# Optimization experiments

Measured on AMD Instinct MI355X. Metric: run time of the kernel, lower is better.

The kernel has to match this reference:

```python
import jax, jax.numpy as jnp
import numpy as np

Q, N_EMBED, DIM = 4, 1024, 256
B, S = 8, 2048


def setup_inputs() -> dict:
    key = jax.random.key(0)
    k1, k2 = jax.random.split(key)
    x = jax.random.normal(k1, (B, S, DIM), dtype=jnp.float32)
    codebooks = jax.random.normal(k2, (Q, N_EMBED, DIM), dtype=jnp.float32)
    return {"x": x, "codebooks": codebooks}


def _vq_lookup(flat, embed):
    # flat: [M, D], embed: [K, D]
    dist = (jnp.sum(flat * flat, axis=-1, keepdims=True)
            - 2.0 * flat @ embed.T
            + jnp.sum(embed * embed, axis=-1))
    idx = jnp.argmin(dist, axis=-1)          # [M]
    quantize = embed[idx]                    # gather: [M, D]
    return quantize, idx


def reference(x, codebooks):
    sg = jax.lax.stop_gradient
    b, s, d = x.shape
    num_q = codebooks.shape[0]
    residual = x
    quantized_output = jnp.zeros_like(x)
    all_indices, all_losses = [], []
    for i in range(num_q):  # small fixed loop over quantizers
        flat = residual.reshape(-1, d)
        q, idx = _vq_lookup(flat, codebooks[i])
        q = q.reshape(b, s, d)
        # commitment loss: mse(sg(quantize), input)
        loss = jnp.mean((sg(q) - residual) ** 2)
        # straight-through estimator
        q_st = residual + sg(q - residual)
        residual = residual - q_st
        quantized_output = quantized_output + q_st
        all_indices.append(idx.reshape(b, s))
        all_losses.append(loss)
    return quantized_output, jnp.stack(all_indices), jnp.stack(all_losses)
```

## Files before the change

kernel.cpp:

```cpp
#include <hip/hip_runtime.h>

#define QQ   4
#define NE   1024
#define DIMD 256
#define MM   16384
#define TM   32
#define NW   8
#define CAP  32

typedef short v8s __attribute__((ext_vector_type(8)));
typedef float v4f __attribute__((ext_vector_type(4)));


__device__ __forceinline__ unsigned short f2bf(float f) {
  unsigned u = __float_as_uint(f);
  return (unsigned short)((u + 0x7FFFu + ((u >> 16) & 1u)) >> 16);
}

__device__ __forceinline__ float np_sumsq_256_x32(const float* __restrict__ p,
                                                  int j) {
  const int bi = j >> 4, L = j & 15;
  const float* q = p + bi * 128 + L;
  float s0 = __fmul_rn(q[0], q[0]);
  float s1 = __fmul_rn(q[16], q[16]);
  float s2 = __fmul_rn(q[32], q[32]);
  float s3 = __fmul_rn(q[48], q[48]);
  float s4 = __fmul_rn(q[64], q[64]);
  float s5 = __fmul_rn(q[80], q[80]);
  float s6 = __fmul_rn(q[96], q[96]);
  float s7 = __fmul_rn(q[112], q[112]);
  float w = __fadd_rn(__fadd_rn(__fadd_rn(s0, s1), __fadd_rn(s2, s3)),
                      __fadd_rn(__fadd_rn(s4, s5), __fadd_rn(s6, s7)));
  float u  = __fadd_rn(w,  __shfl_down(w, 8, 64));
  float t  = __fadd_rn(u,  __shfl_down(u, 4, 64));
  float r2 = __fadd_rn(t,  __shfl_down(t, 2, 64));
  float bb = __fadd_rn(r2, __shfl_down(r2, 1, 64));
  return __fadd_rn(bb, __shfl_down(bb, 16, 64));
}

__device__ __forceinline__ float np_sumsq_256_x16(const float* __restrict__ p,
                                                  int j) {
  float blk[2];
  #pragma unroll
  for (int bi = 0; bi < 2; ++bi) {
    const float* q = p + bi * 128 + j;
    float s0 = __fmul_rn(q[0], q[0]);
    float s1 = __fmul_rn(q[16], q[16]);
    float s2 = __fmul_rn(q[32], q[32]);
    float s3 = __fmul_rn(q[48], q[48]);
    float s4 = __fmul_rn(q[64], q[64]);
    float s5 = __fmul_rn(q[80], q[80]);
    float s6 = __fmul_rn(q[96], q[96]);
    float s7 = __fmul_rn(q[112], q[112]);
    float w = __fadd_rn(__fadd_rn(__fadd_rn(s0, s1), __fadd_rn(s2, s3)),
                        __fadd_rn(__fadd_rn(s4, s5), __fadd_rn(s6, s7)));
    float u  = __fadd_rn(w,  __shfl_down(w, 8, 64));
    float t  = __fadd_rn(u,  __shfl_down(u, 4, 64));
    float r2 = __fadd_rn(t,  __shfl_down(t, 2, 64));
    blk[bi]  = __fadd_rn(r2, __shfl_down(r2, 1, 64));
  }
  return __fadd_rn(blk[0], blk[1]);
}

__device__ __forceinline__ float np_dist_f4(const float* __restrict__ xp,
                                            const float* __restrict__ ep,
                                            float a, float b) {
  float m = 0.f;
  #pragma unroll 16
  for (int d4 = 0; d4 < DIMD / 4; ++d4) {
    const float4 xv = *(const float4*)(xp + d4 * 4);
    const float4 ev = *(const float4*)(ep + d4 * 4);
    m = fmaf(xv.x, ev.x, m);
    m = fmaf(xv.y, ev.y, m);
    m = fmaf(xv.z, ev.z, m);
    m = fmaf(xv.w, ev.w, m);
  }
  return __fadd_rn(__fsub_rn(a, __fmul_rn(2.0f, m)), b);
}

__global__ __launch_bounds__(256) void k_prep(const float* __restrict__ cb,
                                              unsigned short* __restrict__ cb16,
                                              float* __restrict__ bK,
                                              double* __restrict__ lossP,
                                              unsigned* __restrict__ done) {
  const int g = blockIdx.x * 256 + threadIdx.x;
  {
    const int i = g * 4;
    float4 f = *(const float4*)(cb + i);
    unsigned short t[4] = {f2bf(f.x), f2bf(f.y), f2bf(f.z), f2bf(f.w)};
    *(short4*)(cb16 + i) = *(short4*)t;
  }
  if (g < QQ * NE * 32) {
    const int row = g >> 5, j = g & 31;
    float b = np_sumsq_256_x32(cb + (size_t)row * DIMD, j);
    if (j == 0) bK[row] = b;
  }
  if (g < QQ * 64) lossP[g] = 0.0;
  if (g == 0) *done = 0u;
}

__global__ __launch_bounds__(512, 2) void k_fused(
    const float* __restrict__ x,
    const unsigned short* __restrict__ cb16a,
    const float* __restrict__ cba,
    const float* __restrict__ bKa,
    double* __restrict__ lossP,
    unsigned* __restrict__ doneCnt,
    float* __restrict__ out_q,
    float* __restrict__ idx_out,
    float* __restrict__ out_loss) {
  __shared__ float residF[TM][DIMD + 4];
  __shared__ unsigned short sX[TM][DIMD + 8];
  __shared__ float  sBK[NE];
  __shared__ float  av_s[TM];
  __shared__ float  candD[TM][NW];
  __shared__ float  thrS[TM];
  __shared__ int    cnt[TM];
  __shared__ int    candL[TM][CAP];
  __shared__ float  dcD[TM][CAP];
  __shared__ int    bcode[TM];
  __shared__ float  fwD[NW];
  __shared__ int    fwI[NW];
  __shared__ double lossW[NW];

  const int tid  = threadIdx.x;
  const int lane = tid & 63;
  const int wv   = tid >> 6;
  const int rowBase = blockIdx.x * TM;
  const int r16 = tid >> 4;
  const int j16 = tid & 15;
  const int d0  = j16 * 16;
  const int m16  = lane & 15;
  const int quad = lane >> 4;

  {
    const float* xp = x + (size_t)(rowBase + r16) * DIMD + d0;
    #pragma unroll
    for (int h = 0; h < 4; ++h)
      *(float4*)&residF[r16][d0 + h * 4] = *(const float4*)(xp + h * 4);
  }
  __syncthreads();

  #pragma unroll 1
  for (int qi = 0; qi < QQ; ++qi) {
    const unsigned short* cb16 = cb16a + (size_t)qi * NE * DIMD;
    const float* cb = cba + (size_t)qi * NE * DIMD;
    const float* bK = bKa + (size_t)qi * NE;

    {
      float av = np_sumsq_256_x16(&residF[r16][0], j16);
      if (j16 == 0) av_s[r16] = av;
    }
    if (tid < TM) cnt[tid] = 0;
    sBK[tid] = bK[tid];
    sBK[tid + 512] = bK[tid + 512];
    {
      #pragma unroll
      for (int h = 0; h < 2; ++h) {
        const float* rp = &residF[r16][d0 + h * 8];
        const float4 f0 = *(const float4*)rp;
        const float4 f1 = *(const float4*)(rp + 4);
        unsigned short t[8] = {f2bf(f0.x), f2bf(f0.y), f2bf(f0.z), f2bf(f0.w),
                               f2bf(f1.x), f2bf(f1.y), f2bf(f1.z), f2bf(f1.w)};
        *(v8s*)&sX[r16][d0 + h * 8] = *(v8s*)t;
      }
    }
    __syncthreads();

    float bmx;
    {
      float bm = sBK[lane];
      #pragma unroll
      for (int t = 1; t < 16; ++t) bm = fmaxf(bm, sBK[lane + t * 64]);
      #pragma unroll
      for (int off = 32; off; off >>= 1) bm = fmaxf(bm, __shfl_xor(bm, off, 64));
      bmx = bm;
    }

    v4f acc[2][8];
    #pragma unroll
    for (int mt = 0; mt < 2; ++mt)
      #pragma unroll
      for (int ct = 0; ct < 8; ++ct) acc[mt][ct] = (v4f)(0.f);
    const unsigned short* bptr =
        cb16 + ((size_t)(wv * 128 + m16)) * DIMD + quad * 8;
    #pragma unroll
    for (int kc = 0; kc < 8; ++kc) {
      v8s bfr[8];
      #pragma unroll
      for (int ct = 0; ct < 8; ++ct)
        bfr[ct] = *(const v8s*)(bptr + (size_t)ct * 16 * DIMD + kc * 32);
      v8s a0 = *(const v8s*)&sX[m16][kc * 32 + quad * 8];
      v8s a1 = *(const v8s*)&sX[16 + m16][kc * 32 + quad * 8];
      #pragma unroll
      for (int ct = 0; ct < 8; ++ct) {
        acc[0][ct] = __builtin_amdgcn_mfma_f32_16x16x32_bf16(a0, bfr[ct], acc[0][ct], 0, 0, 0);
        acc[1][ct] = __builtin_amdgcn_mfma_f32_16x16x32_bf16(a1, bfr[ct], acc[1][ct], 0, 0, 0);
      }
    }

    float av8[2][4];
    #pragma unroll
    for (int mt = 0; mt < 2; ++mt)
      #pragma unroll
      for (int v = 0; v < 4; ++v) av8[mt][v] = av_s[mt * 16 + quad * 4 + v];
    #pragma unroll
    for (int ct = 0; ct < 8; ++ct) {
      const float bv = sBK[wv * 128 + ct * 16 + m16];
      #pragma unroll
      for (int mt = 0; mt < 2; ++mt)
        #pragma unroll
        for (int v = 0; v < 4; ++v)
          acc[mt][ct][v] = av8[mt][v] - 2.0f * acc[mt][ct][v] + bv;
    }

    #pragma unroll
    for (int mt = 0; mt < 2; ++mt) {
      float vmin[4];
      #pragma unroll
      for (int v = 0; v < 4; ++v) {
        vmin[v] = acc[mt][0][v];
        #pragma unroll
        for (int ct = 1; ct < 8; ++ct) vmin[v] = fminf(vmin[v], acc[mt][ct][v]);
        #pragma unroll
        for (int off = 1; off < 16; off <<= 1)
          vmin[v] = fminf(vmin[v], __shfl_xor(vmin[v], off, 64));
      }
      if (m16 == 0) {
        #pragma unroll
        for (int v = 0; v < 4; ++v) candD[mt * 16 + quad * 4 + v][wv] = vmin[v];
      }
    }
    __syncthreads();
    if (tid < TM) {
      float bd = candD[tid][0];
      #pragma unroll
      for (int w = 1; w < NW; ++w) bd = fminf(bd, candD[tid][w]);
      thrS[tid] = bd + 0.03125f * sqrtf(av_s[tid] * bmx) + 0.1f;
    }
    __syncthreads();

    #pragma unroll
    for (int ct = 0; ct < 8; ++ct) {
      const int code = wv * 128 + ct * 16 + m16;
      #pragma unroll
      for (int mt = 0; mt < 2; ++mt) {
        #pragma unroll
        for (int v = 0; v < 4; ++v) {
          const int row = mt * 16 + quad * 4 + v;
          if (acc[mt][ct][v] <= thrS[row]) {
            int pos = atomicAdd(&cnt[row], 1);
            if (pos < CAP) candL[row][pos] = code;
          }
        }
      }
    }
    __syncthreads();

    {
      const int n = (cnt[r16] <= CAP) ? cnt[r16] : 0;
      if (j16 < n) {
        const int code = candL[r16][j16];
        dcD[r16][j16] = np_dist_f4(&residF[r16][0], cb + (size_t)code * DIMD,
                                   av_s[r16], sBK[code]);
      }
      if (j16 + 16 < n) {
        const int code = candL[r16][j16 + 16];
        dcD[r16][j16 + 16] = np_dist_f4(&residF[r16][0], cb + (size_t)code * DIMD,
                                        av_s[r16], sBK[code]);
      }
    }
    __syncthreads();

    for (int r = 0; r < TM; ++r) {
      if (cnt[r] > CAP) {
        const float* xp = &residF[r][0];
        const float a = av_s[r];
        float d1 = np_dist_f4(xp, cb + (size_t)tid * DIMD, a, sBK[tid]);
        float d2 = np_dist_f4(xp, cb + (size_t)(tid + 512) * DIMD, a, sBK[tid + 512]);
        int i1 = tid;
        if (d2 < d1) { d1 = d2; i1 = tid + 512; }
        #pragma unroll
        for (int off = 32; off; off >>= 1) {
          float vd = __shfl_xor(d1, off, 64);
          int vi = __shfl_xor(i1, off, 64);
          if (vd < d1 || (vd == d1 && vi < i1)) { d1 = vd; i1 = vi; }
        }
        if (lane == 0) { fwD[wv] = d1; fwI[wv] = i1; }
        __syncthreads();
        if (tid == 0) {
          float bd = fwD[0];
          int bi = fwI[0];
          #pragma unroll
          for (int w = 1; w < NW; ++w) {
            if (fwD[w] < bd || (fwD[w] == bd && fwI[w] < bi)) {
              bd = fwD[w]; bi = fwI[w];
            }
          }
          bcode[r] = bi;
        }
        __syncthreads();
      }
    }

    if (tid < TM) {
      if (cnt[tid] <= CAP) {
        float bd = 3.4e38f;
        int bi = 0x7fffffff;
        for (int ci = 0; ci < cnt[tid]; ++ci) {
          float d = dcD[tid][ci];
          int code = candL[tid][ci];
          if (d < bd || (d == bd && code < bi)) { bd = d; bi = code; }
        }
        bcode[tid] = bi;
      }
      idx_out[(size_t)qi * MM + rowBase + tid] = (float)bcode[tid];
    }
    __syncthreads();

    const int codeB = bcode[r16];
    double lsum = 0.0;
    #pragma unroll
    for (int h = 0; h < 4; ++h) {
      const int d = d0 + h * 4;
      const float4 ev = *(const float4*)(cb + (size_t)codeB * DIMD + d);
      const float4 rv = *(const float4*)&residF[r16][d];
      float t0 = __fsub_rn(ev.x, rv.x), u0 = __fadd_rn(rv.x, t0);
      float t1 = __fsub_rn(ev.y, rv.y), u1 = __fadd_rn(rv.y, t1);
      float t2 = __fsub_rn(ev.z, rv.z), u2 = __fadd_rn(rv.z, t2);
      float t3 = __fsub_rn(ev.w, rv.w), u3 = __fadd_rn(rv.w, t3);
      *(float4*)&residF[r16][d] =
          make_float4(__fsub_rn(rv.x, u0), __fsub_rn(rv.y, u1),
                      __fsub_rn(rv.z, u2), __fsub_rn(rv.w, u3));
      lsum += (double)__fmul_rn(t0, t0) + (double)__fmul_rn(t1, t1) +
              (double)__fmul_rn(t2, t2) + (double)__fmul_rn(t3, t3);
    }
    #pragma unroll
    for (int off = 32; off; off >>= 1) lsum += __shfl_xor(lsum, off, 64);
    if (lane == 0) lossW[wv] = lsum;
    __syncthreads();
    if (tid == 0) {
      double s = 0.0;
      #pragma unroll
      for (int w = 0; w < NW; ++w) s += lossW[w];
      atomicAdd(lossP + (size_t)qi * 64 + (blockIdx.x & 63), s);
    }
  }

  {
    const float* xp = x + (size_t)(rowBase + r16) * DIMD + d0;
    float* op = out_q + (size_t)(rowBase + r16) * DIMD + d0;
    #pragma unroll
    for (int h = 0; h < 4; ++h) {
      const float4 a = *(const float4*)(xp + h * 4);
      const float4 b = *(const float4*)&residF[r16][d0 + h * 4];
      *(float4*)(op + h * 4) =
          make_float4(__fsub_rn(a.x, b.x), __fsub_rn(a.y, b.y),
                      __fsub_rn(a.z, b.z), __fsub_rn(a.w, b.w));
    }
  }

  __syncthreads();
  if (tid == 0) {
    __threadfence();
    unsigned old = atomicAdd(doneCnt, 1u);
    cnt[0] = (old == (unsigned)(gridDim.x - 1)) ? 1 : 0;
  }
  __syncthreads();
  if (cnt[0] && tid < 64) {
    const int qi2 = tid >> 4;
    double s = 0.0;
    #pragma unroll
    for (int i = 0; i < 4; ++i)
      s += atomicAdd(lossP + (size_t)qi2 * 64 + (tid & 15) * 4 + i, 0.0);
    #pragma unroll
    for (int off = 8; off; off >>= 1) s += __shfl_down(s, off, 16);
    if ((tid & 15) == 0)
      out_loss[qi2] = (float)(s * (1.0 / (double)((size_t)MM * DIMD)));
  }
}

extern "C" void kernel_launch(void* const* d_in, const int* in_sizes, int n_in,
                              void* d_out, int out_size, void* d_ws, size_t ws_size,
                              hipStream_t stream) {
  const float* x = (const float*)d_in[0];
  const float* cb = (const float*)d_in[1];
  float* ws = (float*)d_ws;
  unsigned short* cb16 = (unsigned short*)ws;
  float* bK = ws + 524288;
  double* lossP = (double*)(ws + 528384);
  unsigned* done = (unsigned*)(ws + 528896);

  float* out = (float*)d_out;
  float* out_idx = out + (size_t)MM * DIMD;
  float* out_loss = out_idx + (size_t)QQ * MM;

  k_prep<<<dim3(1024), dim3(256), 0, stream>>>(cb, cb16, bK, lossP, done);
  k_fused<<<dim3(MM / TM), dim3(512), 0, stream>>>(x, cb16, cb, bK, lossP,
                                                   done, out, out_idx, out_loss);
}
```

Baseline: 323.3 us.

## Double threads per block to 1024, splitting codebook across 16 waves

Raises the block to 1024 threads (16 waves). Each wave now covers 64 codebook entries instead of 128, and each thread handles 8 dims of a row instead of 16, with the row, candidate and fallback work remapped to match. This halves per-wave accumulator and fragment registers so more waves can be resident to hide codebook load latency. In exchange, block-wide barriers now synchronise more waves, and the launch-bounds request of 4 blocks of 1024 threads may force register spilling.

```diff
diff --git a/kernel.cpp b/kernel.cpp
--- a/kernel.cpp
+++ b/kernel.cpp
@@ -5,7 +5,7 @@
 #define DIMD 256
 #define MM   16384
 #define TM   32
-#define NW   8
+#define NW   16
 #define CAP  32
 
 typedef short v8s __attribute__((ext_vector_type(8)));
@@ -38,30 +38,6 @@
   return __fadd_rn(bb, __shfl_down(bb, 16, 64));
 }
 
-__device__ __forceinline__ float np_sumsq_256_x16(const float* __restrict__ p,
-                                                  int j) {
-  float blk[2];
-  #pragma unroll
-  for (int bi = 0; bi < 2; ++bi) {
-    const float* q = p + bi * 128 + j;
-    float s0 = __fmul_rn(q[0], q[0]);
-    float s1 = __fmul_rn(q[16], q[16]);
-    float s2 = __fmul_rn(q[32], q[32]);
-    float s3 = __fmul_rn(q[48], q[48]);
-    float s4 = __fmul_rn(q[64], q[64]);
-    float s5 = __fmul_rn(q[80], q[80]);
-    float s6 = __fmul_rn(q[96], q[96]);
-    float s7 = __fmul_rn(q[112], q[112]);
-    float w = __fadd_rn(__fadd_rn(__fadd_rn(s0, s1), __fadd_rn(s2, s3)),
-                        __fadd_rn(__fadd_rn(s4, s5), __fadd_rn(s6, s7)));
-    float u  = __fadd_rn(w,  __shfl_down(w, 8, 64));
-    float t  = __fadd_rn(u,  __shfl_down(u, 4, 64));
-    float r2 = __fadd_rn(t,  __shfl_down(t, 2, 64));
-    blk[bi]  = __fadd_rn(r2, __shfl_down(r2, 1, 64));
-  }
-  return __fadd_rn(blk[0], blk[1]);
-}
-
 __device__ __forceinline__ float np_dist_f4(const float* __restrict__ xp,
                                             const float* __restrict__ ep,
                                             float a, float b) {
@@ -99,7 +75,7 @@
   if (g == 0) *done = 0u;
 }
 
-__global__ __launch_bounds__(512, 2) void k_fused(
+__global__ __launch_bounds__(1024, 4) void k_fused(
     const float* __restrict__ x,
     const unsigned short* __restrict__ cb16a,
     const float* __restrict__ cba,
@@ -127,17 +103,16 @@
   const int lane = tid & 63;
   const int wv   = tid >> 6;
   const int rowBase = blockIdx.x * TM;
-  const int r16 = tid >> 4;
-  const int j16 = tid & 15;
-  const int d0  = j16 * 16;
+  const int r32 = tid >> 5;
+  const int j32 = tid & 31;
+  const int d0  = j32 * 8;
   const int m16  = lane & 15;
   const int quad = lane >> 4;
 
   {
-    const float* xp = x + (size_t)(rowBase + r16) * DIMD + d0;
-    #pragma unroll
-    for (int h = 0; h < 4; ++h)
-      *(float4*)&residF[r16][d0 + h * 4] = *(const float4*)(xp + h * 4);
+    const float* xp = x + (size_t)(rowBase + r32) * DIMD + d0;
+    *(float4*)&residF[r32][d0]     = *(const float4*)xp;
+    *(float4*)&residF[r32][d0 + 4] = *(const float4*)(xp + 4);
   }
   __syncthreads();
 
@@ -148,22 +123,18 @@
     const float* bK = bKa + (size_t)qi * NE;
 
     {
-      float av = np_sumsq_256_x16(&residF[r16][0], j16);
-      if (j16 == 0) av_s[r16] = av;
+      float av = np_sumsq_256_x32(&residF[r32][0], j32);
+      if (j32 == 0) av_s[r32] = av;
     }
     if (tid < TM) cnt[tid] = 0;
-    sBK[tid] = bK[tid];
-    sBK[tid + 512] = bK[tid + 512];
+    if (tid < NE) sBK[tid] = bK[tid];
     {
-      #pragma unroll
-      for (int h = 0; h < 2; ++h) {
-        const float* rp = &residF[r16][d0 + h * 8];
-        const float4 f0 = *(const float4*)rp;
-        const float4 f1 = *(const float4*)(rp + 4);
-        unsigned short t[8] = {f2bf(f0.x), f2bf(f0.y), f2bf(f0.z), f2bf(f0.w),
-                               f2bf(f1.x), f2bf(f1.y), f2bf(f1.z), f2bf(f1.w)};
-        *(v8s*)&sX[r16][d0 + h * 8] = *(v8s*)t;
-      }
+      const float* rp = &residF[r32][d0];
+      const float4 f0 = *(const float4*)rp;
+      const float4 f1 = *(const float4*)(rp + 4);
+      unsigned short t[8] = {f2bf(f0.x), f2bf(f0.y), f2bf(f0.z), f2bf(f0.w),
+                             f2bf(f1.x), f2bf(f1.y), f2bf(f1.z), f2bf(f1.w)};
+      *(v8s*)&sX[r32][d0] = *(v8s*)t;
     }
     __syncthreads();
 
@@ -177,23 +148,23 @@
       bmx = bm;
     }
 
-    v4f acc[2][8];
+    v4f acc[2][4];
     #pragma unroll
     for (int mt = 0; mt < 2; ++mt)
       #pragma unroll
-      for (int ct = 0; ct < 8; ++ct) acc[mt][ct] = (v4f)(0.f);
+      for (int ct = 0; ct < 4; ++ct) acc[mt][ct] = (v4f)(0.f);
     const unsigned short* bptr =
-        cb16 + ((size_t)(wv * 128 + m16)) * DIMD + quad * 8;
+        cb16 + ((size_t)(wv * 64 + m16)) * DIMD + quad * 8;
     #pragma unroll
     for (int kc = 0; kc < 8; ++kc) {
-      v8s bfr[8];
-      #pragma unroll
-      for (int ct = 0; ct < 8; ++ct)
+      v8s bfr[4];
+      #pragma unroll
+      for (int ct = 0; ct < 4; ++ct)
         bfr[ct] = *(const v8s*)(bptr + (size_t)ct * 16 * DIMD + kc * 32);
       v8s a0 = *(const v8s*)&sX[m16][kc * 32 + quad * 8];
       v8s a1 = *(const v8s*)&sX[16 + m16][kc * 32 + quad * 8];
       #pragma unroll
-      for (int ct = 0; ct < 8; ++ct) {
+      for (int ct = 0; ct < 4; ++ct) {
         acc[0][ct] = __builtin_amdgcn_mfma_f32_16x16x32_bf16(a0, bfr[ct], acc[0][ct], 0, 0, 0);
         acc[1][ct] = __builtin_amdgcn_mfma_f32_16x16x32_bf16(a1, bfr[ct], acc[1][ct], 0, 0, 0);
       }
@@ -205,8 +176,8 @@
       #pragma unroll
       for (int v = 0; v < 4; ++v) av8[mt][v] = av_s[mt * 16 + quad * 4 + v];
     #pragma unroll
-    for (int ct = 0; ct < 8; ++ct) {
-      const float bv = sBK[wv * 128 + ct * 16 + m16];
+    for (int ct = 0; ct < 4; ++ct) {
+      const float bv = sBK[wv * 64 + ct * 16 + m16];
       #pragma unroll
       for (int mt = 0; mt < 2; ++mt)
         #pragma unroll
@@ -221,7 +192,7 @@
       for (int v = 0; v < 4; ++v) {
         vmin[v] = acc[mt][0][v];
         #pragma unroll
-        for (int ct = 1; ct < 8; ++ct) vmin[v] = fminf(vmin[v], acc[mt][ct][v]);
+        for (int ct = 1; ct < 4; ++ct) vmin[v] = fminf(vmin[v], acc[mt][ct][v]);
         #pragma unroll
         for (int off = 1; off < 16; off <<= 1)
           vmin[v] = fminf(vmin[v], __shfl_xor(vmin[v], off, 64));
@@ -241,8 +212,8 @@
     __syncthreads();
 
     #pragma unroll
-    for (int ct = 0; ct < 8; ++ct) {
-      const int code = wv * 128 + ct * 16 + m16;
+    for (int ct = 0; ct < 4; ++ct) {
+      const int code = wv * 64 + ct * 16 + m16;
       #pragma unroll
       for (int mt = 0; mt < 2; ++mt) {
         #pragma unroll
@@ -258,16 +229,11 @@
     __syncthreads();
 
     {
-      const int n = (cnt[r16] <= CAP) ? cnt[r16] : 0;
-      if (j16 < n) {
-        const int code = candL[r16][j16];
-        dcD[r16][j16] = np_dist_f4(&residF[r16][0], cb + (size_t)code * DIMD,
-                                   av_s[r16], sBK[code]);
-      }
-      if (j16 + 16 < n) {
-        const int code = candL[r16][j16 + 16];
-        dcD[r16][j16 + 16] = np_dist_f4(&residF[r16][0], cb + (size_t)code * DIMD,
-                                        av_s[r16], sBK[code]);
+      const int n = (cnt[r32] <= CAP) ? cnt[r32] : 0;
+      if (j32 < n) {
+        const int code = candL[r32][j32];
+        dcD[r32][j32] = np_dist_f4(&residF[r32][0], cb + (size_t)code * DIMD,
+                                   av_s[r32], sBK[code]);
       }
     }
     __syncthreads();
@@ -277,9 +243,7 @@
         const float* xp = &residF[r][0];
         const float a = av_s[r];
         float d1 = np_dist_f4(xp, cb + (size_t)tid * DIMD, a, sBK[tid]);
-        float d2 = np_dist_f4(xp, cb + (size_t)(tid + 512) * DIMD, a, sBK[tid + 512]);
         int i1 = tid;
-        if (d2 < d1) { d1 = d2; i1 = tid + 512; }
         #pragma unroll
         for (int off = 32; off; off >>= 1) {
           float vd = __shfl_xor(d1, off, 64);
@@ -318,18 +282,18 @@
     }
     __syncthreads();
 
-    const int codeB = bcode[r16];
+    const int codeB = bcode[r32];
     double lsum = 0.0;
     #pragma unroll
-    for (int h = 0; h < 4; ++h) {
+    for (int h = 0; h < 2; ++h) {
       const int d = d0 + h * 4;
       const float4 ev = *(const float4*)(cb + (size_t)codeB * DIMD + d);
-      const float4 rv = *(const float4*)&residF[r16][d];
+      const float4 rv = *(const float4*)&residF[r32][d];
       float t0 = __fsub_rn(ev.x, rv.x), u0 = __fadd_rn(rv.x, t0);
       float t1 = __fsub_rn(ev.y, rv.y), u1 = __fadd_rn(rv.y, t1);
       float t2 = __fsub_rn(ev.z, rv.z), u2 = __fadd_rn(rv.z, t2);
       float t3 = __fsub_rn(ev.w, rv.w), u3 = __fadd_rn(rv.w, t3);
-      *(float4*)&residF[r16][d] =
+      *(float4*)&residF[r32][d] =
           make_float4(__fsub_rn(rv.x, u0), __fsub_rn(rv.y, u1),
                       __fsub_rn(rv.z, u2), __fsub_rn(rv.w, u3));
       lsum += (double)__fmul_rn(t0, t0) + (double)__fmul_rn(t1, t1) +
@@ -348,16 +312,16 @@
   }
 
   {
-    const float* xp = x + (size_t)(rowBase + r16) * DIMD + d0;
-    float* op = out_q + (size_t)(rowBase + r16) * DIMD + d0;
-    #pragma unroll
-    for (int h = 0; h < 4; ++h) {
-      const float4 a = *(const float4*)(xp + h * 4);
-      const float4 b = *(const float4*)&residF[r16][d0 + h * 4];
-      *(float4*)(op + h * 4) =
-          make_float4(__fsub_rn(a.x, b.x), __fsub_rn(a.y, b.y),
-                      __fsub_rn(a.z, b.z), __fsub_rn(a.w, b.w));
-    }
+    const float* xp = x + (size_t)(rowBase + r32) * DIMD + d0;
+    float* op = out_q + (size_t)(rowBase + r32) * DIMD + d0;
+    const float4 a0 = *(const float4*)xp;
+    const float4 a1 = *(const float4*)(xp + 4);
+    const float4 b0 = *(const float4*)&residF[r32][d0];
+    const float4 b1 = *(const float4*)&residF[r32][d0 + 4];
+    *(float4*)op = make_float4(__fsub_rn(a0.x, b0.x), __fsub_rn(a0.y, b0.y),
+                               __fsub_rn(a0.z, b0.z), __fsub_rn(a0.w, b0.w));
+    *(float4*)(op + 4) = make_float4(__fsub_rn(a1.x, b1.x), __fsub_rn(a1.y, b1.y),
+                                     __fsub_rn(a1.z, b1.z), __fsub_rn(a1.w, b1.w));
   }
 
   __syncthreads();
@@ -396,6 +360,6 @@
   float* out_loss = out_idx + (size_t)QQ * MM;
 
   k_prep<<<dim3(1024), dim3(256), 0, stream>>>(cb, cb16, bK, lossP, done);
-  k_fused<<<dim3(MM / TM), dim3(512), 0, stream>>>(x, cb16, cb, bK, lossP,
-                                                   done, out, out_idx, out_loss);
-}
+  k_fused<<<dim3(MM / TM), dim3(1024), 0, stream>>>(x, cb16, cb, bK, lossP,
+                                                    done, out, out_idx, out_loss);
+}
```

New measurement: 344.6 us. 1.07x slower.

## Double rows per block to reuse each codebook fragment across four M-tiles

Applied to the files above, without the earlier changes.

Raises the row tile from 32 to 64 rows per block. Each wave now runs MFMAs for four 16-row sub-tiles against every loaded bf16 codebook fragment, which halves codebook reads per row. Threads are remapped to 8 per row, and shared memory moves into a dynamically sized struct so the larger footprint fits. In exchange the grid halves to 256 blocks, so each CU likely gets a single block, and accumulator registers double, which risks spills and weaker latency hiding.

```diff
diff --git a/kernel.cpp b/kernel.cpp
--- a/kernel.cpp
+++ b/kernel.cpp
@@ -4,13 +4,29 @@
 #define NE   1024
 #define DIMD 256
 #define MM   16384
-#define TM   32
+#define TM   64
 #define NW   8
 #define CAP  32
 
 typedef short v8s __attribute__((ext_vector_type(8)));
 typedef float v4f __attribute__((ext_vector_type(4)));
 
+
+struct SLds {
+  double lossW[NW];
+  float  residF[TM][DIMD + 4];
+  unsigned short sX[TM][DIMD + 8];
+  float  sBK[NE];
+  float  av_s[TM];
+  float  candD[TM][NW];
+  float  thrS[TM];
+  int    cnt[TM];
+  int    candL[TM][CAP];
+  float  dcD[TM][CAP];
+  int    bcode[TM];
+  float  fwD[NW];
+  int    fwI[NW];
+};
 
 __device__ __forceinline__ unsigned short f2bf(float f) {
   unsigned u = __float_as_uint(f);
@@ -38,23 +54,28 @@
   return __fadd_rn(bb, __shfl_down(bb, 16, 64));
 }
 
-__device__ __forceinline__ float np_sumsq_256_x16(const float* __restrict__ p,
-                                                  int j) {
+__device__ __forceinline__ float np_sumsq_256_x8(const float* __restrict__ p,
+                                                 int j) {
   float blk[2];
   #pragma unroll
   for (int bi = 0; bi < 2; ++bi) {
-    const float* q = p + bi * 128 + j;
-    float s0 = __fmul_rn(q[0], q[0]);
-    float s1 = __fmul_rn(q[16], q[16]);
-    float s2 = __fmul_rn(q[32], q[32]);
-    float s3 = __fmul_rn(q[48], q[48]);
-    float s4 = __fmul_rn(q[64], q[64]);
-    float s5 = __fmul_rn(q[80], q[80]);
-    float s6 = __fmul_rn(q[96], q[96]);
-    float s7 = __fmul_rn(q[112], q[112]);
-    float w = __fadd_rn(__fadd_rn(__fadd_rn(s0, s1), __fadd_rn(s2, s3)),
-                        __fadd_rn(__fadd_rn(s4, s5), __fadd_rn(s6, s7)));
-    float u  = __fadd_rn(w,  __shfl_down(w, 8, 64));
+    const float* base = p + bi * 128;
+    float wpair[2];
+    #pragma unroll
+    for (int h = 0; h < 2; ++h) {
+      const float* q = base + j + h * 8;
+      float s0 = __fmul_rn(q[0], q[0]);
+      float s1 = __fmul_rn(q[16], q[16]);
+      float s2 = __fmul_rn(q[32], q[32]);
+      float s3 = __fmul_rn(q[48], q[48]);
+      float s4 = __fmul_rn(q[64], q[64]);
+      float s5 = __fmul_rn(q[80], q[80]);
+      float s6 = __fmul_rn(q[96], q[96]);
+      float s7 = __fmul_rn(q[112], q[112]);
+      wpair[h] = __fadd_rn(__fadd_rn(__fadd_rn(s0, s1), __fadd_rn(s2, s3)),
+                           __fadd_rn(__fadd_rn(s4, s5), __fadd_rn(s6, s7)));
+    }
+    float u  = __fadd_rn(wpair[0], wpair[1]);
     float t  = __fadd_rn(u,  __shfl_down(u, 4, 64));
     float r2 = __fadd_rn(t,  __shfl_down(t, 2, 64));
     blk[bi]  = __fadd_rn(r2, __shfl_down(r2, 1, 64));
@@ -109,35 +130,24 @@
     float* __restrict__ out_q,
     float* __restrict__ idx_out,
     float* __restrict__ out_loss) {
-  __shared__ float residF[TM][DIMD + 4];
-  __shared__ unsigned short sX[TM][DIMD + 8];
-  __shared__ float  sBK[NE];
-  __shared__ float  av_s[TM];
-  __shared__ float  candD[TM][NW];
-  __shared__ float  thrS[TM];
-  __shared__ int    cnt[TM];
-  __shared__ int    candL[TM][CAP];
-  __shared__ float  dcD[TM][CAP];
-  __shared__ int    bcode[TM];
-  __shared__ float  fwD[NW];
-  __shared__ int    fwI[NW];
-  __shared__ double lossW[NW];
+  extern __shared__ char smem_raw[];
+  SLds& S = *reinterpret_cast<SLds*>(smem_raw);
 
   const int tid  = threadIdx.x;
   const int lane = tid & 63;
   const int wv   = tid >> 6;
   const int rowBase = blockIdx.x * TM;
-  const int r16 = tid >> 4;
-  const int j16 = tid & 15;
-  const int d0  = j16 * 16;
+  const int r8  = tid >> 3;
+  const int j8  = tid & 7;
+  const int c0  = j8 * 32;
   const int m16  = lane & 15;
   const int quad = lane >> 4;
 
   {
-    const float* xp = x + (size_t)(rowBase + r16) * DIMD + d0;
-    #pragma unroll
-    for (int h = 0; h < 4; ++h)
-      *(float4*)&residF[r16][d0 + h * 4] = *(const float4*)(xp + h * 4);
+    const float* xp = x + (size_t)(rowBase + r8) * DIMD + c0;
+    #pragma unroll
+    for (int h = 0; h < 8; ++h)
+      *(float4*)&S.residF[r8][c0 + h * 4] = *(const float4*)(xp + h * 4);
   }
   __syncthreads();
 
@@ -148,38 +158,38 @@
     const float* bK = bKa + (size_t)qi * NE;
 
     {
-      float av = np_sumsq_256_x16(&residF[r16][0], j16);
-      if (j16 == 0) av_s[r16] = av;
-    }
-    if (tid < TM) cnt[tid] = 0;
-    sBK[tid] = bK[tid];
-    sBK[tid + 512] = bK[tid + 512];
+      float av = np_sumsq_256_x8(&S.residF[r8][0], j8);
+      if (j8 == 0) S.av_s[r8] = av;
+    }
+    if (tid < TM) S.cnt[tid] = 0;
+    S.sBK[tid] = bK[tid];
+    S.sBK[tid + 512] = bK[tid + 512];
     {
       #pragma unroll
-      for (int h = 0; h < 2; ++h) {
-        const float* rp = &residF[r16][d0 + h * 8];
+      for (int h = 0; h < 4; ++h) {
+        const float* rp = &S.residF[r8][c0 + h * 8];
         const float4 f0 = *(const float4*)rp;
         const float4 f1 = *(const float4*)(rp + 4);
         unsigned short t[8] = {f2bf(f0.x), f2bf(f0.y), f2bf(f0.z), f2bf(f0.w),
                                f2bf(f1.x), f2bf(f1.y), f2bf(f1.z), f2bf(f1.w)};
-        *(v8s*)&sX[r16][d0 + h * 8] = *(v8s*)t;
+        *(v8s*)&S.sX[r8][c0 + h * 8] = *(v8s*)t;
       }
     }
     __syncthreads();
 
     float bmx;
     {
-      float bm = sBK[lane];
-      #pragma unroll
-      for (int t = 1; t < 16; ++t) bm = fmaxf(bm, sBK[lane + t * 64]);
+      float bm = S.sBK[lane];
+      #pragma unroll
+      for (int t = 1; t < 16; ++t) bm = fmaxf(bm, S.sBK[lane + t * 64]);
       #pragma unroll
       for (int off = 32; off; off >>= 1) bm = fmaxf(bm, __shfl_xor(bm, off, 64));
       bmx = bm;
     }
 
-    v4f acc[2][8];
-    #pragma unroll
-    for (int mt = 0; mt < 2; ++mt)
+    v4f acc[4][8];
+    #pragma unroll
+    for (int mt = 0; mt < 4; ++mt)
       #pragma unroll
       for (int ct = 0; ct < 8; ++ct) acc[mt][ct] = (v4f)(0.f);
     const unsigned short* bptr =
@@ -190,32 +200,36 @@
       #pragma unroll
       for (int ct = 0; ct < 8; ++ct)
         bfr[ct] = *(const v8s*)(bptr + (size_t)ct * 16 * DIMD + kc * 32);
-      v8s a0 = *(const v8s*)&sX[m16][kc * 32 + quad * 8];
-      v8s a1 = *(const v8s*)&sX[16 + m16][kc * 32 + quad * 8];
+      v8s afr[4];
+      #pragma unroll
+      for (int mt = 0; mt < 4; ++mt)
+        afr[mt] = *(const v8s*)&S.sX[mt * 16 + m16][kc * 32 + quad * 8];
       #pragma unroll
       for (int ct = 0; ct < 8; ++ct) {
-        acc[0][ct] = __builtin_amdgcn_mfma_f32_16x16x32_bf16(a0, bfr[ct], acc[0][ct], 0, 0, 0);
-        acc[1][ct] = __builtin_amdgcn_mfma_f32_16x16x32_bf16(a1, bfr[ct], acc[1][ct], 0, 0, 0);
-      }
-    }
-
-    float av8[2][4];
-    #pragma unroll
-    for (int mt = 0; mt < 2; ++mt)
-      #pragma unroll
-      for (int v = 0; v < 4; ++v) av8[mt][v] = av_s[mt * 16 + quad * 4 + v];
+        #pragma unroll
+        for (int mt = 0; mt < 4; ++mt)
+          acc[mt][ct] = __builtin_amdgcn_mfma_f32_16x16x32_bf16(
+              afr[mt], bfr[ct], acc[mt][ct], 0, 0, 0);
+      }
+    }
+
+    float av16[4][4];
+    #pragma unroll
+    for (int mt = 0; mt < 4; ++mt)
+      #pragma unroll
+      for (int v = 0; v < 4; ++v) av16[mt][v] = S.av_s[mt * 16 + quad * 4 + v];
     #pragma unroll
     for (int ct = 0; ct < 8; ++ct) {
-      const float bv = sBK[wv * 128 + ct * 16 + m16];
-      #pragma unroll
-      for (int mt = 0; mt < 2; ++mt)
+      const float bv = S.sBK[wv * 128 + ct * 16 + m16];
+      #pragma unroll
+      for (int mt = 0; mt < 4; ++mt)
         #pragma unroll
         for (int v = 0; v < 4; ++v)
-          acc[mt][ct][v] = av8[mt][v] - 2.0f * acc[mt][ct][v] + bv;
-    }
-
-    #pragma unroll
-    for (int mt = 0; mt < 2; ++mt) {
+          acc[mt][ct][v] = av16[mt][v] - 2.0f * acc[mt][ct][v] + bv;
+    }
+
+    #pragma unroll
+    for (int mt = 0; mt < 4; ++mt) {
       float vmin[4];
       #pragma unroll
       for (int v = 0; v < 4; ++v) {
@@ -228,15 +242,16 @@
       }
       if (m16 == 0) {
         #pragma unroll
-        for (int v = 0; v < 4; ++v) candD[mt * 16 + quad * 4 + v][wv] = vmin[v];
+        for (int v = 0; v < 4; ++v)
+          S.candD[mt * 16 + quad * 4 + v][wv] = vmin[v];
       }
     }
     __syncthreads();
     if (tid < TM) {
-      float bd = candD[tid][0];
-      #pragma unroll
-      for (int w = 1; w < NW; ++w) bd = fminf(bd, candD[tid][w]);
-      thrS[tid] = bd + 0.03125f * sqrtf(av_s[tid] * bmx) + 0.1f;
+      float bd = S.candD[tid][0];
+      #pragma unroll
+      for (int w = 1; w < NW; ++w) bd = fminf(bd, S.candD[tid][w]);
+      S.thrS[tid] = bd + 0.03125f * sqrtf(S.av_s[tid] * bmx) + 0.1f;
     }
     __syncthreads();
 
@@ -244,13 +259,13 @@
     for (int ct = 0; ct < 8; ++ct) {
       const int code = wv * 128 + ct * 16 + m16;
       #pragma unroll
-      for (int mt = 0; mt < 2; ++mt) {
+      for (int mt = 0; mt < 4; ++mt) {
         #pragma unroll
         for (int v = 0; v < 4; ++v) {
           const int row = mt * 16 + quad * 4 + v;
-          if (acc[mt][ct][v] <= thrS[row]) {
-            int pos = atomicAdd(&cnt[row], 1);
-            if (pos < CAP) candL[row][pos] = code;
+          if (acc[mt][ct][v] <= S.thrS[row]) {
+            int pos = atomicAdd(&S.cnt[row], 1);
+            if (pos < CAP) S.candL[row][pos] = code;
           }
         }
       }
@@ -258,26 +273,26 @@
     __syncthreads();
 
     {
-      const int n = (cnt[r16] <= CAP) ? cnt[r16] : 0;
-      if (j16 < n) {
-        const int code = candL[r16][j16];
-        dcD[r16][j16] = np_dist_f4(&residF[r16][0], cb + (size_t)code * DIMD,
-                                   av_s[r16], sBK[code]);
-      }
-      if (j16 + 16 < n) {
-        const int code = candL[r16][j16 + 16];
-        dcD[r16][j16 + 16] = np_dist_f4(&residF[r16][0], cb + (size_t)code * DIMD,
-                                        av_s[r16], sBK[code]);
+      const int n = (S.cnt[r8] <= CAP) ? S.cnt[r8] : 0;
+      #pragma unroll
+      for (int s = 0; s < 4; ++s) {
+        const int ci = j8 + s * 8;
+        if (ci < n) {
+          const int code = S.candL[r8][ci];
+          S.dcD[r8][ci] = np_dist_f4(&S.residF[r8][0],
+                                     cb + (size_t)code * DIMD,
+                                     S.av_s[r8], S.sBK[code]);
+        }
       }
     }
     __syncthreads();
 
     for (int r = 0; r < TM; ++r) {
-      if (cnt[r] > CAP) {
-        const float* xp = &residF[r][0];
-        const float a = av_s[r];
-        float d1 = np_dist_f4(xp, cb + (size_t)tid * DIMD, a, sBK[tid]);
-        float d2 = np_dist_f4(xp, cb + (size_t)(tid + 512) * DIMD, a, sBK[tid + 512]);
+      if (S.cnt[r] > CAP) {
+        const float* xp = &S.residF[r][0];
+        const float a = S.av_s[r];
+        float d1 = np_dist_f4(xp, cb + (size_t)tid * DIMD, a, S.sBK[tid]);
+        float d2 = np_dist_f4(xp, cb + (size_t)(tid + 512) * DIMD, a, S.sBK[tid + 512]);
         int i1 = tid;
         if (d2 < d1) { d1 = d2; i1 = tid + 512; }
         #pragma unroll
@@ -286,50 +301,50 @@
           int vi = __shfl_xor(i1, off, 64);
           if (vd < d1 || (vd == d1 && vi < i1)) { d1 = vd; i1 = vi; }
         }
-        if (lane == 0) { fwD[wv] = d1; fwI[wv] = i1; }
+        if (lane == 0) { S.fwD[wv] = d1; S.fwI[wv] = i1; }
         __syncthreads();
         if (tid == 0) {
-          float bd = fwD[0];
-          int bi = fwI[0];
+          float bd = S.fwD[0];
+          int bi = S.fwI[0];
           #pragma unroll
           for (int w = 1; w < NW; ++w) {
-            if (fwD[w] < bd || (fwD[w] == bd && fwI[w] < bi)) {
-              bd = fwD[w]; bi = fwI[w];
+            if (S.fwD[w] < bd || (S.fwD[w] == bd && S.fwI[w] < bi)) {
+              bd = S.fwD[w]; bi = S.fwI[w];
             }
           }
-          bcode[r] = bi;
+          S.bcode[r] = bi;
         }
         __syncthreads();
       }
     }
 
     if (tid < TM) {
-      if (cnt[tid] <= CAP) {
+      if (S.cnt[tid] <= CAP) {
         float bd = 3.4e38f;
         int bi = 0x7fffffff;
-        for (int ci = 0; ci < cnt[tid]; ++ci) {
-          float d = dcD[tid][ci];
-          int code = candL[tid][ci];
+        for (int ci = 0; ci < S.cnt[tid]; ++ci) {
+          float d = S.dcD[tid][ci];
+          int code = S.candL[tid][ci];
           if (d < bd || (d == bd && code < bi)) { bd = d; bi = code; }
         }
-        bcode[tid] = bi;
-      }
-      idx_out[(size_t)qi * MM + rowBase + tid] = (float)bcode[tid];
-    }
-    __syncthreads();
-
-    const int codeB = bcode[r16];
+        S.bcode[tid] = bi;
+      }
+      idx_out[(size_t)qi * MM + rowBase + tid] = (float)S.bcode[tid];
+    }
+    __syncthreads();
+
+    const int codeB = S.bcode[r8];
     double lsum = 0.0;
     #pragma unroll
-    for (int h = 0; h < 4; ++h) {
-      const int d = d0 + h * 4;
+    for (int h = 0; h < 8; ++h) {
+      const int d = c0 + h * 4;
       const float4 ev = *(const float4*)(cb + (size_t)codeB * DIMD + d);
-      const float4 rv = *(const float4*)&residF[r16][d];
+      const float4 rv = *(const float4*)&S.residF[r8][d];
       float t0 = __fsub_rn(ev.x, rv.x), u0 = __fadd_rn(rv.x, t0);
       float t1 = __fsub_rn(ev.y, rv.y), u1 = __fadd_rn(rv.y, t1);
       float t2 = __fsub_rn(ev.z, rv.z), u2 = __fadd_rn(rv.z, t2);
       float t3 = __fsub_rn(ev.w, rv.w), u3 = __fadd_rn(rv.w, t3);
-      *(float4*)&residF[r16][d] =
+      *(float4*)&S.residF[r8][d] =
           make_float4(__fsub_rn(rv.x, u0), __fsub_rn(rv.y, u1),
                       __fsub_rn(rv.z, u2), __fsub_rn(rv.w, u3));
       lsum += (double)__fmul_rn(t0, t0) + (double)__fmul_rn(t1, t1) +
@@ -337,23 +352,23 @@
     }
     #pragma unroll
     for (int off = 32; off; off >>= 1) lsum += __shfl_xor(lsum, off, 64);
-    if (lane == 0) lossW[wv] = lsum;
+    if (lane == 0) S.lossW[wv] = lsum;
     __syncthreads();
     if (tid == 0) {
       double s = 0.0;
       #pragma unroll
-      for (int w = 0; w < NW; ++w) s += lossW[w];
+      for (int w = 0; w < NW; ++w) s += S.lossW[w];
       atomicAdd(lossP + (size_t)qi * 64 + (blockIdx.x & 63), s);
     }
   }
 
   {
-    const float* xp = x + (size_t)(rowBase + r16) * DIMD + d0;
-    float* op = out_q + (size_t)(rowBase + r16) * DIMD + d0;
-    #pragma unroll
-    for (int h = 0; h < 4; ++h) {
+    const float* xp = x + (size_t)(rowBase + r8) * DIMD + c0;
+    float* op = out_q + (size_t)(rowBase + r8) * DIMD + c0;
+    #pragma unroll
+    for (int h = 0; h < 8; ++h) {
       const float4 a = *(const float4*)(xp + h * 4);
-      const float4 b = *(const float4*)&residF[r16][d0 + h * 4];
+      const float4 b = *(const float4*)&S.residF[r8][c0 + h * 4];
       *(float4*)(op + h * 4) =
           make_float4(__fsub_rn(a.x, b.x), __fsub_rn(a.y, b.y),
                       __fsub_rn(a.z, b.z), __fsub_rn(a.w, b.w));
@@ -364,10 +379,10 @@
   if (tid == 0) {
     __threadfence();
     unsigned old = atomicAdd(doneCnt, 1u);
-    cnt[0] = (old == (unsigned)(gridDim.x - 1)) ? 1 : 0;
+    S.cnt[0] = (old == (unsigned)(gridDim.x - 1)) ? 1 : 0;
   }
   __syncthreads();
-  if (cnt[0] && tid < 64) {
+  if (S.cnt[0] && tid < 64) {
     const int qi2 = tid >> 4;
     double s = 0.0;
     #pragma unroll
@@ -395,7 +410,15 @@
   float* out_idx = out + (size_t)MM * DIMD;
   float* out_loss = out_idx + (size_t)QQ * MM;
 
+  static bool attr_set = false;
+  if (!attr_set) {
+    hipFuncSetAttribute(reinterpret_cast<const void*>(k_fused),
+                        hipFuncAttributeMaxDynamicSharedMemorySize,
+                        (int)sizeof(SLds));
+    attr_set = true;
+  }
+
   k_prep<<<dim3(1024), dim3(256), 0, stream>>>(cb, cb16, bK, lossP, done);
-  k_fused<<<dim3(MM / TM), dim3(512), 0, stream>>>(x, cb16, cb, bK, lossP,
-                                                   done, out, out_idx, out_loss);
-}
+  k_fused<<<dim3(MM / TM), dim3(512), sizeof(SLds), stream>>>(
+      x, cb16, cb, bK, lossP, done, out, out_idx, out_loss);
+}
```

Measured after the change: 331.7 us. +2.6%, slower.
